# Kernel optimization log

Measured on AMD Instinct MI355X. Metric: run time of the kernel, lower is better.

Reference implementation:

```python
import jax, jax.numpy as jnp
import numpy as np

N = 50000      # nodes
E = 800000     # edges
GENE = 64      # gene_dim
HID = 128      # hidden_dim
NCLS = 10      # num_classes
EPS = 1e-5


def setup_inputs() -> dict:
    key = jax.random.key(0)
    ks = jax.random.split(key, 4)
    inp = {
        "x": jax.random.normal(ks[0], (N, GENE), jnp.float32),
        "edge_index": jax.random.randint(ks[1], (2, E), 0, N),
    }
    # PNA-style conv: concat([x, 4 aggregators x 3 scalers]) -> 13*d_in features
    dims = [(GENE, HID), (HID, 2 * HID), (2 * HID, HID), (HID, HID // 2)]
    for i, (din, dout) in enumerate(dims, 1):
        k = jax.random.fold_in(key, i)
        inp[f"W{i}"] = jax.random.normal(k, (13 * din, dout), jnp.float32) / float(np.sqrt(13 * din))
        inp[f"b{i}"] = jnp.zeros((dout,), jnp.float32)
        inp[f"gamma{i}"] = jnp.ones((dout,), jnp.float32)
        inp[f"beta{i}"] = jnp.zeros((dout,), jnp.float32)
    inp["Wc"] = jax.random.normal(ks[2], (HID // 2, NCLS), jnp.float32) / float(np.sqrt(HID // 2))
    inp["bc"] = jnp.zeros((NCLS,), jnp.float32)
    return inp


def _pna(x, src, dst, deg, log_deg, delta, W, b):
    # gather source features along edges: [E, d]
    msg = x[src]
    cnt = jnp.maximum(deg, 1.0)[:, None]
    s = jax.ops.segment_sum(msg, dst, num_segments=N)
    mean = s / cnt
    mean_sq = jax.ops.segment_sum(msg * msg, dst, num_segments=N) / cnt
    std = jnp.sqrt(jnp.maximum(mean_sq - mean * mean, 0.0) + EPS)
    has = (deg > 0)[:, None]
    mn = jnp.where(has, jax.ops.segment_min(msg, dst, num_segments=N), 0.0)
    mx = jnp.where(has, jax.ops.segment_max(msg, dst, num_segments=N), 0.0)
    aggs = jnp.concatenate([mean, mn, mx, std], axis=-1)  # [N, 4d]
    amp = (log_deg / delta)[:, None]                       # amplification scaler
    att = jnp.where(log_deg > 0, delta / jnp.maximum(log_deg, 1e-6), 1.0)[:, None]
    feat = jnp.concatenate([x, aggs, aggs * amp, aggs * att], axis=-1)  # [N, 13d]
    return feat @ W + b


def _bn(h, gamma, beta):
    m = h.mean(axis=0)
    v = h.var(axis=0)
    return (h - m) / jnp.sqrt(v + EPS) * gamma + beta


def reference(x, edge_index, W1, b1, gamma1, beta1, W2, b2, gamma2, beta2,
              W3, b3, gamma3, beta3, W4, b4, gamma4, beta4, Wc, bc):
    src, dst = edge_index[0], edge_index[1]
    deg = jax.ops.segment_sum(jnp.ones((E,), jnp.float32), dst, num_segments=N)
    log_deg = jnp.log1p(deg)
    delta = log_deg.mean()
    h = _pna(x, src, dst, deg, log_deg, delta, W1, b1)
    h = _bn(jax.nn.relu(h), gamma1, beta1)
    h = _pna(h, src, dst, deg, log_deg, delta, W2, b2)
    h = _bn(jax.nn.relu(h), gamma2, beta2)
    h = _pna(h, src, dst, deg, log_deg, delta, W3, b3)
    h = _bn(jax.nn.relu(h), gamma3, beta3)
    h = _pna(h, src, dst, deg, log_deg, delta, W4, b4)
    h = _bn(jax.nn.relu(h), gamma4, beta4)
    return h @ Wc + bc
```

## Files before the change

kernel.cpp:

```cpp
#include <hip/hip_runtime.h>
#include <hip/hip_bf16.h>

#define NN 50000
#define NE 800000
#define EPSV 1e-5f
#define NB 49

typedef _Float16 h8 __attribute__((ext_vector_type(8)));
typedef float    f4 __attribute__((ext_vector_type(4)));

#define AS1 __attribute__((address_space(1)))
#define AS3 __attribute__((address_space(3)))

__device__ __forceinline__ void gload_lds16(const _Float16* g, _Float16* l){
  __builtin_amdgcn_global_load_lds((const AS1 void*)g, (AS3 void*)l, 16, 0, 0);
}


__global__ void k_deg(const int* __restrict__ dst, int* __restrict__ deg){
  int e = blockIdx.x*blockDim.x + threadIdx.x;
  if(e < NE) atomicAdd(&deg[dst[e]], 1);
}

__global__ void k_logdeg(const int* __restrict__ deg, float* __restrict__ logdeg,
                         float* __restrict__ dsum){
  int i = blockIdx.x*blockDim.x + threadIdx.x;
  float v = 0.f;
  if(i < NN){ v = log1pf((float)deg[i]); logdeg[i] = v; }
  __shared__ float sh[256];
  sh[threadIdx.x] = v; __syncthreads();
  for(int off=128; off>0; off>>=1){
    if(threadIdx.x < off) sh[threadIdx.x] += sh[threadIdx.x+off];
    __syncthreads();
  }
  if(threadIdx.x == 0) atomicAdd(dsum, sh[0]);
}

__global__ void k_scalers(const float* __restrict__ logdeg, const float* __restrict__ dsum,
                          float* __restrict__ amp, float* __restrict__ att){
  int i = blockIdx.x*blockDim.x + threadIdx.x;
  if(i >= NN) return;
  float delta = dsum[0] / (float)NN;
  float ld = logdeg[i];
  amp[i] = ld / delta;
  att[i] = (ld > 0.f) ? (delta / fmaxf(ld, 1e-6f)) : 1.f;
}

__global__ void k_scan1(const int* __restrict__ deg, int* __restrict__ rowptr,
                        int* __restrict__ bsum){
  __shared__ int buf[1024];
  int tid = threadIdx.x;
  int i = blockIdx.x*1024 + tid;
  int v = (i < NN) ? deg[i] : 0;
  buf[tid] = v; __syncthreads();
  for(int off=1; off<1024; off<<=1){
    int t = (tid >= off) ? buf[tid-off] : 0;
    __syncthreads();
    buf[tid] += t;
    __syncthreads();
  }
  if(i < NN) rowptr[i] = buf[tid] - v;
  if(tid == 1023) bsum[blockIdx.x] = buf[1023];
}

__global__ void k_scan2(int* __restrict__ bsum){
  if(threadIdx.x == 0){
    int s = 0;
    for(int b = 0; b < NB; b++){ int t = bsum[b]; bsum[b] = s; s += t; }
    bsum[NB] = s;
  }
}

__global__ void k_scan3(int* __restrict__ rowptr, int* __restrict__ cursor,
                        const int* __restrict__ bsum){
  int i = blockIdx.x*256 + threadIdx.x;
  if(i < NN){
    int v = rowptr[i] + bsum[i >> 10];
    rowptr[i] = v; cursor[i] = v;
  }
  if(i == NN) rowptr[NN] = bsum[NB];
}

__global__ void k_fill(const int* __restrict__ src, const int* __restrict__ dst,
                       int* __restrict__ cursor, int* __restrict__ colidx){
  int e = blockIdx.x*blockDim.x + threadIdx.x;
  if(e < NE){
    int pos = atomicAdd(&cursor[dst[e]], 1);
    colidx[pos] = src[e];
  }
}

__global__ void k_cvtx(const float* __restrict__ x, _Float16* __restrict__ act){
  int i = blockIdx.x*256 + threadIdx.x;
  if(i < NN*64) act[i] = (_Float16)x[i];
}

__global__ void k_coef_id(float* __restrict__ cs, float* __restrict__ csh,
                          _Float16* __restrict__ cs16, _Float16* __restrict__ csh16){
  int c = threadIdx.x;
  cs[c] = 1.f; csh[c] = 0.f;
  cs16[c] = (_Float16)1.f; csh16[c] = (_Float16)0.f;
}

__global__ void k_bn_coef(const float* __restrict__ colsum, const float* __restrict__ colss,
                          const float* __restrict__ gamma, const float* __restrict__ beta,
                          int dout, float* __restrict__ cs, float* __restrict__ csh,
                          _Float16* __restrict__ cs16, _Float16* __restrict__ csh16){
  int c = threadIdx.x;
  if(c >= dout) return;
  float mean = colsum[c] / (float)NN;
  float var  = colss[c] / (float)NN - mean*mean;
  float inv  = rsqrtf(fmaxf(var, 0.f) + EPSV);
  float a = inv * gamma[c];
  float b = beta[c] - mean * a;
  cs[c] = a; csh[c] = b;
  cs16[c] = (_Float16)a; csh16[c] = (_Float16)b;
}


template<int D>
__global__ __launch_bounds__(256) void k_agg8(
    const _Float16* __restrict__ act,
    const int* __restrict__ rowptr, const int* __restrict__ colidx,
    const float* __restrict__ cs, const float* __restrict__ csh,
    _Float16* __restrict__ aggs, size_t aggN)
{
  constexpr int LPN = D >> 3;
  constexpr int NPW = 64 / LPN;
  int wv = threadIdx.x >> 6, lane = threadIdx.x & 63;
  int n = blockIdx.x*(NPW*4) + wv*NPW + (lane / LPN);
  int c = (lane % LPN) * 8;
  if(n >= NN) return;
  int beg = rowptr[n], end = rowptr[n+1];
  const _Float16* hp = act + c;

  float s[8], q[8], mn[8], mx[8];
  #pragma unroll
  for(int j = 0; j < 8; j++){ s[j]=0.f; q[j]=0.f; mn[j]=INFINITY; mx[j]=-INFINITY; }

#define ACC8(v) { _Pragma("unroll") for(int j=0;j<8;j++){ float a=(float)(v)[j]; \
    s[j]+=a; q[j]+=a*a; mn[j]=fminf(mn[j],a); mx[j]=fmaxf(mx[j],a); } }

  int e = beg;
  for(; e+8 <= end; e+=8){
    int i0=colidx[e],   i1=colidx[e+1], i2=colidx[e+2], i3=colidx[e+3];
    int i4=colidx[e+4], i5=colidx[e+5], i6=colidx[e+6], i7=colidx[e+7];
    h8 v0 = *(const h8*)(hp + (size_t)i0*D);
    h8 v1 = *(const h8*)(hp + (size_t)i1*D);
    h8 v2 = *(const h8*)(hp + (size_t)i2*D);
    h8 v3 = *(const h8*)(hp + (size_t)i3*D);
    h8 v4 = *(const h8*)(hp + (size_t)i4*D);
    h8 v5 = *(const h8*)(hp + (size_t)i5*D);
    h8 v6 = *(const h8*)(hp + (size_t)i6*D);
    h8 v7 = *(const h8*)(hp + (size_t)i7*D);
    ACC8(v0) ACC8(v1) ACC8(v2) ACC8(v3) ACC8(v4) ACC8(v5) ACC8(v6) ACC8(v7)
  }
  for(; e+4 <= end; e+=4){
    int i0=colidx[e], i1=colidx[e+1], i2=colidx[e+2], i3=colidx[e+3];
    h8 v0 = *(const h8*)(hp + (size_t)i0*D);
    h8 v1 = *(const h8*)(hp + (size_t)i1*D);
    h8 v2 = *(const h8*)(hp + (size_t)i2*D);
    h8 v3 = *(const h8*)(hp + (size_t)i3*D);
    ACC8(v0) ACC8(v1) ACC8(v2) ACC8(v3)
  }
  for(; e < end; e++){
    h8 v = *(const h8*)(hp + (size_t)colidx[e]*D);
    ACC8(v)
  }
#undef ACC8

  float cnt = (end>beg) ? (float)(end-beg) : 1.f;
  h8 vm, vn, vx, vs;
  #pragma unroll
  for(int j = 0; j < 8; j++){
    float a = cs[c+j], b = csh[c+j];
    float mean_r = s[j]/cnt;
    float var_r  = fmaxf(q[j]/cnt - mean_r*mean_r, 0.f);
    float meanp = a*mean_r + b;
    float mnp = (a >= 0.f) ? a*mn[j]+b : a*mx[j]+b;
    float mxp = (a >= 0.f) ? a*mx[j]+b : a*mn[j]+b;
    float sdp = sqrtf(a*a*var_r + EPSV);
    if(end <= beg){ meanp = 0.f; mnp = 0.f; mxp = 0.f; sdp = sqrtf(EPSV); }
    vm[j] = (_Float16)meanp; vn[j] = (_Float16)mnp;
    vx[j] = (_Float16)mxp;   vs[j] = (_Float16)sdp;
  }

  _Float16* dst = aggs + (size_t)(c>>6)*aggN + (size_t)n*256 + (c & 63);
  *(h8*)(dst)       = vm;
  *(h8*)(dst + 64)  = vn;
  *(h8*)(dst + 128) = vx;
  *(h8*)(dst + 192) = vs;
}


struct PackJob { const float* W; _Float16* dst; int d, o, j0, start; };
struct PackArgs { PackJob job[9]; int total; };

__global__ void k_pack_all(PackArgs a){
  int idx = blockIdx.x*256 + threadIdx.x;
  if(idx >= a.total) return;
  int ji = 0;
  while(ji < 8 && idx >= a.job[ji+1].start) ji++;
  PackJob J = a.job[ji];
  int rel = idx - J.start;
  int j    = rel & 7;
  int lane = (rel >> 3) & 63;
  int rem  = rel >> 9;
  int ntiles = J.o >> 4;
  int kb = rem / ntiles;
  int nt = rem - kb*ntiles;
  int k = kb*32 + (lane>>4)*8 + j;
  int n = nt*16 + (lane&15);
  int srcrow;
  if(k < 64)       srcrow = J.j0 + k;
  else if(k < 320){ int t=k-64;  srcrow = (1+(t>>6))*J.d + J.j0 + (t&63); }
  else if(k < 576){ int t=k-320; srcrow = (5+(t>>6))*J.d + J.j0 + (t&63); }
  else            { int t=k-576; srcrow = (9+(t>>6))*J.d + J.j0 + (t&63); }
  J.dst[rel] = (_Float16)J.W[(size_t)srcrow*J.o + n];
}


template<int NCH>
__global__ __launch_bounds__(256) void k_mfma_fused(
    const _Float16* __restrict__ actIn,
    const _Float16* __restrict__ aggs,
    const float* __restrict__ amp, const float* __restrict__ att,
    const _Float16* __restrict__ cs16, const _Float16* __restrict__ csh16,
    const _Float16* __restrict__ Wp, int o,
    const float* __restrict__ bias,
    _Float16* __restrict__ out,
    float* __restrict__ colsum, float* __restrict__ colss,
    size_t aggN)
{
  constexpr int D = NCH * 64;
  constexpr int NPH = NCH * 9;
  __shared__ _Float16 Bsm[2][12*512];
  __shared__ float redS[64], redQ[64];
  int tid  = threadIdx.x;
  int wv   = tid >> 6;
  int lane = tid & 63;
  int mi   = lane & 15;
  int q    = lane >> 4;
  int m0   = blockIdx.y * 128 + wv * 32;
  int c0   = blockIdx.x * 64;
  int ntiles = o >> 4;
  int nt0  = blockIdx.x * 4;

  if(tid < 64){ redS[tid] = 0.f; redQ[tid] = 0.f; }

  int mrow[2];
  mrow[0] = min(m0 + mi,      NN-1);
  mrow[1] = min(m0 + 16 + mi, NN-1);
  _Float16 am16[2] = { (_Float16)amp[mrow[0]], (_Float16)amp[mrow[1]] };
  _Float16 at16[2] = { (_Float16)att[mrow[0]], (_Float16)att[mrow[1]] };
  const _Float16* hAb[2];
  const _Float16* agb[2];
  hAb[0] = actIn + (size_t)mrow[0]*D + q*8;
  hAb[1] = actIn + (size_t)mrow[1]*D + q*8;
  agb[0] = aggs + (size_t)mrow[0]*256 + q*8;
  agb[1] = aggs + (size_t)mrow[1]*256 + q*8;

  f4 acc[2][4] = {};

  auto stageX = [&](_Float16* buf, int c){
    const _Float16* Wpc = Wp + (size_t)c*832*o;
    #pragma unroll
    for(int s = 0; s < 2; s++){
      int ti = wv*2 + s;
      int kb = ti >> 2, nn = ti & 3;
      gload_lds16(Wpc + (((size_t)kb*ntiles + nt0 + nn)*64 + lane)*8,
                  buf + ti*512);
    }
  };
  auto stageP = [&](_Float16* buf, int c, int idx){
    const _Float16* Wpc = Wp + (size_t)c*832*o;
    #pragma unroll
    for(int s = 0; s < 3; s++){
      int ti = wv*3 + s;
      int kj = ti >> 2, nn = ti & 3;
      int kb = (kj == 0 ? 2 : (kj == 1 ? 10 : 18)) + idx;
      gload_lds16(Wpc + (((size_t)kb*ntiles + nt0 + nn)*64 + lane)*8,
                  buf + ti*512);
    }
  };

  h8 pA[4]; h8 pS[2]; h8 pH[2];
  auto loadA = [&](int c, int sub){
    if(sub == 0){
      #pragma unroll
      for(int kb = 0; kb < 2; kb++){
        pS[kb] = *(const h8*)(cs16  + c*64 + kb*32 + q*8);
        pH[kb] = *(const h8*)(csh16 + c*64 + kb*32 + q*8);
        #pragma unroll
        for(int t = 0; t < 2; t++)
          pA[kb*2+t] = *(const h8*)(hAb[t] + c*64 + kb*32);
      }
    } else {
      int idx = sub - 1;
      #pragma unroll
      for(int t = 0; t < 2; t++)
        pA[t] = *(const h8*)(agb[t] + (size_t)c*aggN + idx*32);
    }
  };

  stageX(&Bsm[0][0], 0);
  loadA(0, 0);
  __syncthreads();

  #pragma unroll
  for(int ph = 0; ph < NPH; ph++){
    const int c   = ph / 9;
    const int sub = ph % 9;
    _Float16* cur = &Bsm[ph & 1][0];
    _Float16* nxt = &Bsm[(ph & 1) ^ 1][0];

    h8 cA[4] = { pA[0], pA[1], pA[2], pA[3] };
    h8 cS[2] = { pS[0], pS[1] };
    h8 cH[2] = { pH[0], pH[1] };

    if(ph + 1 < NPH){
      const int c2   = (ph + 1) / 9;
      const int sub2 = (ph + 1) % 9;
      if(sub2 == 0) stageX(nxt, c2);
      else          stageP(nxt, c2, sub2 - 1);
      loadA(c2, sub2);
    }

    if(sub == 0){
      #pragma unroll
      for(int kb = 0; kb < 2; kb++)
        #pragma unroll
        for(int t = 0; t < 2; t++){
          h8 ax = cA[kb*2+t]*cS[kb] + cH[kb];
          #pragma unroll
          for(int nn = 0; nn < 4; nn++)
            acc[t][nn] = __builtin_amdgcn_mfma_f32_16x16x32_f16(
                ax, *(const h8*)(cur + (kb*4+nn)*512 + lane*8), acc[t][nn], 0,0,0);
        }
    } else {
      #pragma unroll
      for(int t = 0; t < 2; t++){
        h8 apl = cA[t];
        h8 aam = apl * am16[t];
        h8 aat = apl * at16[t];
        #pragma unroll
        for(int nn = 0; nn < 4; nn++){
          acc[t][nn] = __builtin_amdgcn_mfma_f32_16x16x32_f16(
              apl, *(const h8*)(cur + (0*4+nn)*512 + lane*8), acc[t][nn], 0,0,0);
          acc[t][nn] = __builtin_amdgcn_mfma_f32_16x16x32_f16(
              aam, *(const h8*)(cur + (4+nn)*512 + lane*8), acc[t][nn], 0,0,0);
          acc[t][nn] = __builtin_amdgcn_mfma_f32_16x16x32_f16(
              aat, *(const h8*)(cur + (8+nn)*512 + lane*8), acc[t][nn], 0,0,0);
        }
      }
    }

    __syncthreads();
  }

  #pragma unroll
  for(int nn = 0; nn < 4; nn++){
    int n = c0 + nn*16 + mi;
    float bv = bias[n];
    float ps = 0.f, pq = 0.f;
    #pragma unroll
    for(int t = 0; t < 2; t++){
      #pragma unroll
      for(int r = 0; r < 4; r++){
        int m = m0 + t*16 + q*4 + r;
        if(m < NN){
          float v = fmaxf(bv + acc[t][nn][r], 0.f);
          out[(size_t)m*o + n] = (_Float16)v;
          ps += v; pq += v*v;
        }
      }
    }
    ps += __shfl_xor(ps, 16); pq += __shfl_xor(pq, 16);
    ps += __shfl_xor(ps, 32); pq += __shfl_xor(pq, 32);
    if(q == 0){
      atomicAdd(&redS[nn*16 + mi], ps);
      atomicAdd(&redQ[nn*16 + mi], pq);
    }
  }
  __syncthreads();
  if(tid < 64){
    atomicAdd(&colsum[c0 + tid], redS[tid]);
    atomicAdd(&colss[c0 + tid],  redQ[tid]);
  }
}


__global__ __launch_bounds__(256) void k_cls(const _Float16* __restrict__ h,
    const float* __restrict__ cs, const float* __restrict__ csh,
    const float* __restrict__ Wc, const float* __restrict__ bc,
    float* __restrict__ out){
  __shared__ float w[640];
  __shared__ float bb[16];
  __shared__ float sca[64], shb[64];
  int tid = threadIdx.x;
  for(int i = tid; i < 640; i += 256) w[i] = Wc[i];
  if(tid < 10) bb[tid] = bc[tid];
  if(tid < 64){ sca[tid] = cs[tid]; shb[tid] = csh[tid]; }
  __syncthreads();
  int idx = blockIdx.x*256 + tid;
  int n = idx >> 4;
  int c = idx & 15;
  if(n < NN && c < 10){
    float acc = bb[c];
    const _Float16* hp = h + (size_t)n*64;
    #pragma unroll
    for(int k = 0; k < 64; k++)
      acc += ((float)hp[k]*sca[k] + shb[k]) * w[k*10 + c];
    out[(size_t)n*10 + c] = acc;
  }
}


extern "C" void kernel_launch(void* const* d_in, const int* in_sizes, int n_in,
                              void* d_out, int out_size, void* d_ws, size_t ws_size,
                              hipStream_t stream){
  const float* x = (const float*)d_in[0];
  const int* edge = (const int*)d_in[1];
  const int* esrc = edge;
  const int* edst = edge + NE;
  const float* W[4]  = {(const float*)d_in[2],  (const float*)d_in[6],
                        (const float*)d_in[10], (const float*)d_in[14]};
  const float* bb[4] = {(const float*)d_in[3],  (const float*)d_in[7],
                        (const float*)d_in[11], (const float*)d_in[15]};
  const float* gm[4] = {(const float*)d_in[4],  (const float*)d_in[8],
                        (const float*)d_in[12], (const float*)d_in[16]};
  const float* bt[4] = {(const float*)d_in[5],  (const float*)d_in[9],
                        (const float*)d_in[13], (const float*)d_in[17]};
  const float* Wc = (const float*)d_in[18];
  const float* bc = (const float*)d_in[19];
  (void)in_sizes; (void)n_in; (void)out_size; (void)ws_size;

  char* p = (char*)d_ws;
  auto alloc = [&](size_t bytes)->char*{
    char* r = p; p += (bytes + 255) & ~(size_t)255; return r;
  };
  _Float16* act0 = (_Float16*)alloc((size_t)NN*256*2);
  _Float16* act1 = (_Float16*)alloc((size_t)NN*256*2);
  _Float16* aggs = (_Float16*)alloc((size_t)4*NN*256*2);
  int*   deg    = (int*)  alloc((size_t)NN*4);
  float* logdeg = (float*)alloc((size_t)NN*4);
  float* amp    = (float*)alloc((size_t)NN*4);
  float* att    = (float*)alloc((size_t)NN*4);
  int*   rowptr = (int*)  alloc((size_t)(NN+1)*4);
  int*   cursor = (int*)  alloc((size_t)NN*4);
  int*   colidx = (int*)  alloc((size_t)NE*4);
  int*   bsum   = (int*)  alloc((size_t)(NB+1)*4);
  float* colsumL= (float*)alloc(4*256*4);
  float* colssL = (float*)alloc(4*256*4);
  float* dsum   = (float*)alloc(256);
  float*    csA  = (float*)   alloc(256*4);
  float*    cshA = (float*)   alloc(256*4);
  float*    csB  = (float*)   alloc(256*4);
  float*    cshB = (float*)   alloc(256*4);
  _Float16* cs16A  = (_Float16*)alloc(256*2);
  _Float16* csh16A = (_Float16*)alloc(256*2);
  _Float16* cs16B  = (_Float16*)alloc(256*2);
  _Float16* csh16B = (_Float16*)alloc(256*2);

  const int din[4]  = {64, 128, 256, 128};
  const int dto[4]  = {128, 256, 128, 64};
  const size_t aggN = (size_t)NN*256;
  _Float16* WpL[4];
  PackArgs pa; int pj = 0, poff = 0;
  for(int l = 0; l < 4; l++){
    int nch = din[l]/64;
    WpL[l] = (_Float16*)alloc((size_t)nch*832*dto[l]*2);
    for(int c = 0; c < nch; c++){
      pa.job[pj] = { W[l], WpL[l] + (size_t)c*832*dto[l], din[l], dto[l], c*64, poff };
      poff += 832*dto[l]; pj++;
    }
  }
  pa.total = poff;

  hipMemsetAsync(deg, 0, (size_t)NN*4, stream);
  hipMemsetAsync(dsum, 0, 4, stream);
  hipMemsetAsync(colsumL, 0, 4*256*4, stream);
  hipMemsetAsync(colssL,  0, 4*256*4, stream);

  k_pack_all<<<(pa.total+255)/256, 256, 0, stream>>>(pa);
  k_deg     <<<(NE+255)/256, 256, 0, stream>>>(edst, deg);
  k_logdeg  <<<(NN+255)/256, 256, 0, stream>>>(deg, logdeg, dsum);
  k_scalers <<<(NN+255)/256, 256, 0, stream>>>(logdeg, dsum, amp, att);
  k_scan1   <<<NB, 1024, 0, stream>>>(deg, rowptr, bsum);
  k_scan2   <<<1, 64, 0, stream>>>(bsum);
  k_scan3   <<<(NN+256)/256, 256, 0, stream>>>(rowptr, cursor, bsum);
  k_fill    <<<(NE+255)/256, 256, 0, stream>>>(esrc, edst, cursor, colidx);
  k_cvtx    <<<(NN*64+255)/256, 256, 0, stream>>>(x, act0);
  k_coef_id <<<1, 256, 0, stream>>>(csA, cshA, cs16A, csh16A);

  _Float16* actIn = act0;  _Float16* actOut = act1;
  float *csI = csA, *cshI = cshA, *csO = csB, *cshO = cshB;
  _Float16 *cs16I = cs16A, *csh16I = csh16A, *cs16O = cs16B, *csh16O = csh16B;

  for(int l = 0; l < 4; l++){
    int d = din[l], o = dto[l];
    int npb = (64 / (d >> 3)) * 4;
    int nagg = (NN + npb - 1) / npb;
    dim3 g(o/64, (NN+127)/128);
    float* csum = colsumL + l*256;
    float* csq  = colssL + l*256;
    switch(d){
      case 64:
        k_agg8<64><<<nagg, 256, 0, stream>>>(actIn, rowptr, colidx, csI, cshI, aggs, aggN);
        k_mfma_fused<1><<<g, 256, 0, stream>>>(actIn, aggs, amp, att, cs16I, csh16I,
                                               WpL[l], o, bb[l], actOut, csum, csq, aggN);
        break;
      case 128:
        k_agg8<128><<<nagg, 256, 0, stream>>>(actIn, rowptr, colidx, csI, cshI, aggs, aggN);
        k_mfma_fused<2><<<g, 256, 0, stream>>>(actIn, aggs, amp, att, cs16I, csh16I,
                                               WpL[l], o, bb[l], actOut, csum, csq, aggN);
        break;
      default:
        k_agg8<256><<<nagg, 256, 0, stream>>>(actIn, rowptr, colidx, csI, cshI, aggs, aggN);
        k_mfma_fused<4><<<g, 256, 0, stream>>>(actIn, aggs, amp, att, cs16I, csh16I,
                                               WpL[l], o, bb[l], actOut, csum, csq, aggN);
        break;
    }
    k_bn_coef<<<1, 256, 0, stream>>>(csum, csq, gm[l], bt[l], o,
                                     csO, cshO, cs16O, csh16O);
    _Float16* ta = actIn; actIn = actOut; actOut = ta;
    float* tf;
    tf = csI;  csI = csO;  csO = tf;
    tf = cshI; cshI = cshO; cshO = tf;
    _Float16* th;
    th = cs16I;  cs16I = cs16O;  cs16O = th;
    th = csh16I; csh16I = csh16O; csh16O = th;
  }
  k_cls<<<(NN*16+255)/256, 256, 0, stream>>>(actIn, csI, cshI, Wc, bc, (float*)d_out);
}
```

Baseline: 656.0 us.

## Deepen A-operand prefetch, use fine-grained vmcnt barriers, and swizzle block mapping

The fused PNA GEMM kernel now prefetches A-operand registers two phases ahead using a double-banked register set. Full __syncthreads are replaced with hand-written s_waitcnt vmcnt(N)+s_barrier so outstanding prefetch loads are not drained each phase. The MFMA section is wrapped in s_setprio. Block indices are remapped with an XCD-aware swizzle so neighbouring tiles land on the same XCD for L2 reuse. Hand-counted vmcnt values are fragile: a wrong count could read LDS before it is filled, and the extra register bank raises register pressure.

```diff
diff --git a/kernel.cpp b/kernel.cpp
--- a/kernel.cpp
+++ b/kernel.cpp
@@ -241,10 +241,18 @@
   int lane = tid & 63;
   int mi   = lane & 15;
   int q    = lane >> 4;
-  int m0   = blockIdx.y * 128 + wv * 32;
-  int c0   = blockIdx.x * 64;
+
+  int T  = gridDim.x * gridDim.y;
+  int n_ = blockIdx.y * gridDim.x + blockIdx.x;
+  int qq = T >> 3, rr = T & 7, xc = n_ & 7, nl = n_ >> 3;
+  int m_ = (xc < rr ? xc*(qq+1) : rr*(qq+1) + (xc-rr)*qq) + nl;
+  int bx = m_ % gridDim.x;
+  int by = m_ / gridDim.x;
+
+  int m0   = by * 128 + wv * 32;
+  int c0   = bx * 64;
   int ntiles = o >> 4;
-  int nt0  = blockIdx.x * 4;
+  int nt0  = bx * 4;
 
   if(tid < 64){ redS[tid] = 0.f; redQ[tid] = 0.f; }
 
@@ -284,48 +292,59 @@
     }
   };
 
-  h8 pA[4]; h8 pS[2]; h8 pH[2];
-  auto loadA = [&](int c, int sub){
+  h8 pA[2][4]; h8 pS[2][2]; h8 pH[2][2];
+  auto loadA = [&](int ph2, int bank){
+    if(ph2 >= NPH) return;
+    int c = ph2 / 9, sub = ph2 % 9;
     if(sub == 0){
       #pragma unroll
       for(int kb = 0; kb < 2; kb++){
-        pS[kb] = *(const h8*)(cs16  + c*64 + kb*32 + q*8);
-        pH[kb] = *(const h8*)(csh16 + c*64 + kb*32 + q*8);
+        pS[bank][kb] = *(const h8*)(cs16  + c*64 + kb*32 + q*8);
+        pH[bank][kb] = *(const h8*)(csh16 + c*64 + kb*32 + q*8);
         #pragma unroll
         for(int t = 0; t < 2; t++)
-          pA[kb*2+t] = *(const h8*)(hAb[t] + c*64 + kb*32);
+          pA[bank][kb*2+t] = *(const h8*)(hAb[t] + c*64 + kb*32);
       }
     } else {
       int idx = sub - 1;
       #pragma unroll
       for(int t = 0; t < 2; t++)
-        pA[t] = *(const h8*)(agb[t] + (size_t)c*aggN + idx*32);
+        pA[bank][t] = *(const h8*)(agb[t] + (size_t)c*aggN + idx*32);
     }
   };
 
   stageX(&Bsm[0][0], 0);
+  __builtin_amdgcn_sched_barrier(0);
   loadA(0, 0);
-  __syncthreads();
+  loadA(1, 1);
+  asm volatile("s_waitcnt vmcnt(10)\n\ts_barrier" ::: "memory");
 
   #pragma unroll
   for(int ph = 0; ph < NPH; ph++){
-    const int c   = ph / 9;
     const int sub = ph % 9;
+    const int bank = ph & 1;
     _Float16* cur = &Bsm[ph & 1][0];
     _Float16* nxt = &Bsm[(ph & 1) ^ 1][0];
 
-    h8 cA[4] = { pA[0], pA[1], pA[2], pA[3] };
-    h8 cS[2] = { pS[0], pS[1] };
-    h8 cH[2] = { pH[0], pH[1] };
+    h8 cA[4]; h8 cS[2]; h8 cH[2];
+    cA[0] = pA[bank][0]; cA[1] = pA[bank][1];
+    if(sub == 0){
+      cA[2] = pA[bank][2]; cA[3] = pA[bank][3];
+      cS[0] = pS[bank][0]; cS[1] = pS[bank][1];
+      cH[0] = pH[bank][0]; cH[1] = pH[bank][1];
+    }
 
     if(ph + 1 < NPH){
       const int c2   = (ph + 1) / 9;
       const int sub2 = (ph + 1) % 9;
       if(sub2 == 0) stageX(nxt, c2);
       else          stageP(nxt, c2, sub2 - 1);
-      loadA(c2, sub2);
-    }
-
+    }
+    __builtin_amdgcn_sched_barrier(0);
+
+    loadA(ph + 2, bank);
+
+    __builtin_amdgcn_s_setprio(1);
     if(sub == 0){
       #pragma unroll
       for(int kb = 0; kb < 2; kb++)
@@ -354,9 +373,17 @@
         }
       }
     }
-
-    __syncthreads();
-  }
+    __builtin_amdgcn_s_setprio(0);
+
+    if(ph + 1 < NPH){
+      const int ka = (ph + 2 < NPH) ? (((ph + 2) % 9 == 0) ? 8 : 2) : 0;
+      if(ka == 8)      asm volatile("s_waitcnt vmcnt(8)\n\ts_barrier" ::: "memory");
+      else if(ka == 2) asm volatile("s_waitcnt vmcnt(2)\n\ts_barrier" ::: "memory");
+      else             asm volatile("s_waitcnt vmcnt(0)\n\ts_barrier" ::: "memory");
+    }
+  }
+
+  __syncthreads();
 
   #pragma unroll
   for(int nn = 0; nn < 4; nn++){
```

Result: no change. 650.3 us (-0.9%).
